# Kernel optimization log

Hardware: AMD Instinct MI355X
Metric: run time of the kernel (lower is better)

## Reference

```python
import jax, jax.numpy as jnp
import numpy as np

R = 12          # resolution (H = W = G); L = R**3 = 1728
HEADS = 12


def setup_inputs() -> dict:
    key = jax.random.key(0)
    k1, k2, k3 = jax.random.split(key, 3)
    B, L, C = 4, R ** 3, 768
    qkv = jax.random.normal(k1, (3, B, L, C), dtype=jnp.float32)
    lepe_w = jax.random.normal(k2, (C, 1, 3, 3, 3), dtype=jnp.float32) * 0.05
    lepe_b = jax.random.normal(k3, (C,), dtype=jnp.float32) * 0.01
    return {"qkv": qkv, "lepe_w": lepe_w, "lepe_b": lepe_b}


def reference(qkv, lepe_w, lepe_b):
    # qkv: [3, B, L, C]; idx=0 => window == full volume, so attention is dense over L.
    q, k, v = qkv[0], qkv[1], qkv[2]
    B, L, C = q.shape
    hd = C // HEADS
    scale = hd ** -0.5

    # im2cswin with full-volume window preserves token order: [B, L, C] -> [B, H, L, d]
    qh = q.reshape(B, L, HEADS, hd).transpose(0, 2, 1, 3)
    kh = k.reshape(B, L, HEADS, hd).transpose(0, 2, 1, 3)

    # get_lepe: v -> [B, C, R, R, R], depthwise 3x3x3 conv (groups=C)
    v_img = v.transpose(0, 2, 1).reshape(B, C, R, R, R)
    lepe = jax.lax.conv_general_dilated(
        v_img, lepe_w, window_strides=(1, 1, 1), padding="SAME",
        dimension_numbers=("NCDHW", "OIDHW", "NCDHW"), feature_group_count=C,
    ) + lepe_b[None, :, None, None, None]
    lepe = lepe.reshape(B, HEADS, hd, L).transpose(0, 1, 3, 2)   # [B, H, L, d]
    vh = v_img.reshape(B, HEADS, hd, L).transpose(0, 1, 3, 2)    # [B, H, L, d]

    attn = jax.nn.softmax(jnp.einsum("bhqd,bhkd->bhqk", qh * scale, kh), axis=-1)
    out = jnp.einsum("bhqk,bhkd->bhqd", attn, vh) + lepe          # [B, H, L, d]

    # windows2img with full window is an inverse reshape back to [B, L, C]
    return out.transpose(0, 2, 1, 3).reshape(B, L, C)
```

## Files before the change

### kernel.cpp

```cpp
#include <hip/hip_runtime.h>

#define RR 12
#define LL 1728
#define CC 768
#define HEADS 12
#define HD 64
#define BATCH 4

typedef __attribute__((ext_vector_type(8))) short bf8;
typedef __attribute__((ext_vector_type(4))) float f4;

__device__ inline unsigned short f2bf(float x) {
  unsigned int u = __float_as_uint(x);
  return (unsigned short)((u + 0x7FFFu + ((u >> 16) & 1u)) >> 16);
}
__device__ inline unsigned short f2bfr(float x) {
  return (unsigned short)((__float_as_uint(x) + 0x8000u) >> 16);
}

__device__ inline float fast_exp2(float x) {
#if __has_builtin(__builtin_amdgcn_exp2f)
  return __builtin_amdgcn_exp2f(x);
#else
  return exp2f(x);
#endif
}

__device__ inline void gld16(const unsigned short* g, unsigned short* l) {
  __builtin_amdgcn_global_load_lds((const __attribute__((address_space(1))) unsigned int*)g,
                                   (__attribute__((address_space(3))) unsigned int*)l, 16, 0, 0);
}

#define QSCALE 0.1803368801111244f

#define NLEPE 1296
#define NPREP 1296

__global__ __launch_bounds__(256) void combined_kernel(const float* __restrict__ qkv,
                                                       const float* __restrict__ w,
                                                       const float* __restrict__ bias,
                                                       unsigned short* __restrict__ qb,
                                                       unsigned short* __restrict__ kb,
                                                       unsigned short* __restrict__ vT,
                                                       float* __restrict__ out) {
  __shared__ __align__(16) unsigned char smem[27648];
  const int bid = blockIdx.x;
  const int t = threadIdx.x;

  if (bid < NLEPE) {
    const int xg = (bid % 3) * 4;
    const int yg = ((bid / 3) % 3) * 4;
    const int z = (bid / 9) % RR;
    const int ct = (bid / 108) % 3;
    const int b = bid / 324;
    const int c0 = ct * 256;
    const int c = c0 + t;
    float* w_lds = (float*)smem;

    {
      const float* wsrc = w + (size_t)c0 * 27;
#pragma unroll
      for (int i = 0; i < 7; ++i) {
        const int idx = i * 256 + t;
        if (idx < 1728) *(float4*)&w_lds[idx * 4] = *(const float4*)&wsrc[idx * 4];
      }
    }
    __syncthreads();
    float wreg[27];
#pragma unroll
    for (int j = 0; j < 27; ++j) wreg[j] = w_lds[t * 27 + j];

    const float* vb = qkv + ((size_t)(2 * BATCH + b)) * LL * CC + c;
    const float bv = bias[c];
    float acc[4][4];
#pragma unroll
    for (int yy = 0; yy < 4; ++yy)
#pragma unroll
      for (int xx = 0; xx < 4; ++xx) acc[yy][xx] = bv;

#pragma unroll
    for (int dzp = 0; dzp < 3; ++dzp) {
      const int zp = z + dzp - 1;
      const bool zok = (unsigned)zp < RR;
      float vwin[6][6];
#pragma unroll
      for (int wy = 0; wy < 6; ++wy) {
        const int yp = yg - 1 + wy;
        const bool yok = zok & ((unsigned)yp < RR);
        const int rowbase = (zp * RR + yp) * RR;
#pragma unroll
        for (int wx = 0; wx < 6; ++wx) {
          const int xp = xg - 1 + wx;
          const bool ok = yok & ((unsigned)xp < RR);
          const int lp = ok ? rowbase + xp : 0;
          const float vv = vb[(size_t)lp * CC];
          vwin[wy][wx] = ok ? vv : 0.f;
        }
      }
#pragma unroll
      for (int dy = 0; dy < 3; ++dy) {
        const float w0 = wreg[dzp * 9 + dy * 3 + 0];
        const float w1 = wreg[dzp * 9 + dy * 3 + 1];
        const float w2 = wreg[dzp * 9 + dy * 3 + 2];
#pragma unroll
        for (int yy = 0; yy < 4; ++yy) {
#pragma unroll
          for (int xx = 0; xx < 4; ++xx)
            acc[yy][xx] += w0 * vwin[yy + dy][xx] + w1 * vwin[yy + dy][xx + 1] +
                           w2 * vwin[yy + dy][xx + 2];
        }
      }
    }
#pragma unroll
    for (int yy = 0; yy < 4; ++yy) {
      const size_t obase = ((size_t)b * LL + (z * RR + yg + yy) * RR + xg) * CC + c;
#pragma unroll
      for (int xx = 0; xx < 4; ++xx) out[obase + (size_t)xx * CC] = acc[yy][xx];
    }

  } else {
    const int p = bid - NLEPE;
    const int lt = p % 27;
    const int h = (p / 27) % HEADS;
    const int b = p / (27 * HEADS);
    unsigned short* tl = (unsigned short*)smem;

    {
      const int r0 = t >> 4;
      const int c4 = (t & 15) * 4;
#pragma unroll
      for (int pi = 0; pi < 4; ++pi) {
        const int row = lt * 64 + pi * 16 + r0;
        const size_t off = ((size_t)b * LL + row) * CC + h * HD + c4;
        const float4 qv = *(const float4*)(qkv + off);
        ushort4 oq;
        oq.x = f2bf(qv.x * QSCALE); oq.y = f2bf(qv.y * QSCALE);
        oq.z = f2bf(qv.z * QSCALE); oq.w = f2bf(qv.w * QSCALE);
        *(ushort4*)(qb + off) = oq;
        const float4 kv = *(const float4*)(qkv + (size_t)BATCH * LL * CC + off);
        ushort4 ok;
        ok.x = f2bf(kv.x); ok.y = f2bf(kv.y); ok.z = f2bf(kv.z); ok.w = f2bf(kv.w);
        *(ushort4*)(kb + off) = ok;
      }
    }

    const float* vsrc = qkv + ((size_t)(2 * BATCH + b)) * LL * CC;
#pragma unroll
    for (int it = 0; it < 4; ++it) {
      const int idx = it * 256 + t;
      const int lrow = idx >> 4;
      const int c4 = (idx & 15) * 4;
      const float4 vv = *(const float4*)(vsrc + (size_t)(lt * 64 + lrow) * CC + h * HD + c4);
      tl[(c4 + 0) * 65 + lrow] = f2bf(vv.x);
      tl[(c4 + 1) * 65 + lrow] = f2bf(vv.y);
      tl[(c4 + 2) * 65 + lrow] = f2bf(vv.z);
      tl[(c4 + 3) * 65 + lrow] = f2bf(vv.w);
    }
    __syncthreads();
#pragma unroll
    for (int it = 0; it < 4; ++it) {
      const int idx = it * 256 + t;
      const int drow = idx >> 4;
      const int u = idx & 15;
      const int s4 = u * 4;
      const int kbase = (((u >> 3) * 2 + (u & 1)) << 4) + (((u >> 1) & 3) << 2);
      ushort4 o;
      o.x = tl[drow * 65 + kbase + 0];
      o.y = tl[drow * 65 + kbase + 1];
      o.z = tl[drow * 65 + kbase + 2];
      o.w = tl[drow * 65 + kbase + 3];
      *(ushort4*)(vT + (((size_t)(b * HEADS + h) * HD + drow) * LL) + lt * 64 + s4) = o;
    }
  }
}

__global__ __launch_bounds__(512, 3) void attn_kernel(const unsigned short* __restrict__ qb,
                                                      const unsigned short* __restrict__ kb,
                                                      const unsigned short* __restrict__ vT,
                                                      float* __restrict__ out) {
  __shared__ unsigned short k_lds[3][64 * 64];
  __shared__ unsigned short v_lds[3][64 * 64];

  const int g = blockIdx.x;
  const int xcd = g & 7;
  const int ix = g >> 3;
  const int qt = ix % 14;
  const int bh = xcd * 6 + ix / 14;
  const int h = bh % HEADS;
  const int b = bh / HEADS;
  const int stg = (qt * 2) % 27;

  const int t = threadIdx.x;
  const int lane = t & 63;
  const int wave = t >> 6;
  const int m = lane & 15;
  const int quad = lane >> 4;
  const int half = wave >> 2;
  const int qg = wave & 3;

  bf8 qf[2][2];
#pragma unroll
  for (int qsub = 0; qsub < 2; ++qsub) {
    int row = qt * 128 + qg * 32 + qsub * 16 + m;
    row = row < LL ? row : LL - 1;
    const size_t qbase = ((size_t)(b * LL + row)) * CC + h * HD;
    qf[qsub][0] = *(const bf8*)(qb + qbase + quad * 8);
    qf[qsub][1] = *(const bf8*)(qb + qbase + 32 + quad * 8);
  }

  int koff, voff, ldsb;
  {
    const int cidx = wave * 64 + lane;
    const int row = cidx >> 3;
    const int sc = (cidx & 7) ^ (row & 7);
    koff = row * CC + sc * 8;
    voff = row * LL + sc * 8;
    ldsb = wave * 512;
  }

  const unsigned short* kgb = kb + (size_t)b * LL * CC + h * HD;
  const unsigned short* vgb = vT + ((size_t)(b * HEADS + h) * HD) * LL;

#define ISSUE_TILE(KT, BUF)                                                             \
  {                                                                                     \
    gld16(kgb + (size_t)(KT) * (64 * CC) + koff, &k_lds[BUF][ldsb]);                    \
    gld16(vgb + (KT) * 64 + voff, &v_lds[BUF][ldsb]);                                   \
  }

  ISSUE_TILE(stg, 0)
  {
    int k1 = stg + 1; if (k1 >= 27) k1 -= 27;
    ISSUE_TILE(k1, 1)
  }

  f4 o_acc[4][2] = {};
  float psum[2] = {0.f, 0.f};

#define ATTN_BODY(I, STG, WAITN, DOISSUE)                                               \
  {                                                                                     \
    __asm__ volatile("s_waitcnt vmcnt(" #WAITN ")" ::: "memory");                       \
    __builtin_amdgcn_s_barrier();                                                       \
    if (DOISSUE) {                                                                      \
      int ktn = stg + (I) + 2; if (ktn >= 27) ktn -= 27;                                \
      ISSUE_TILE(ktn, ((STG) + 2) % 3)                                                  \
    }                                                                                   \
    f4 s_acc[2][2] = {};                            \
    __builtin_amdgcn_s_setprio(1);                                                      \
    _Pragma("unroll")                                                                   \
    for (int knt = 0; knt < 2; ++knt) {                                                 \
      _Pragma("unroll")                                                                 \
      for (int ksd = 0; ksd < 2; ++ksd) {                                               \
        const int cc = ((ksd * 4 + quad) ^ (m & 7)) * 8;                                \
        const bf8 kf = *(const bf8*)&k_lds[STG][(half * 32 + knt * 16 + m) * 64 + cc];  \
        s_acc[knt][0] = __builtin_amdgcn_mfma_f32_16x16x32_bf16(kf, qf[0][ksd], s_acc[knt][0], 0, 0, 0); \
        s_acc[knt][1] = __builtin_amdgcn_mfma_f32_16x16x32_bf16(kf, qf[1][ksd], s_acc[knt][1], 0, 0, 0); \
      }                                                                                 \
    }                                                                                   \
    __builtin_amdgcn_s_setprio(0);                                                      \
    bf8 pf[2];          \
    _Pragma("unroll")                                                                   \
    for (int qsub = 0; qsub < 2; ++qsub) {                                              \
      union { bf8 v; unsigned int w[4]; } pu;                                           \
      _Pragma("unroll")                                                                 \
      for (int knt = 0; knt < 2; ++knt) {                                               \
        const float p0 = fast_exp2(s_acc[knt][qsub][0]);                                \
        const float p1 = fast_exp2(s_acc[knt][qsub][1]);                                \
        const float p2 = fast_exp2(s_acc[knt][qsub][2]);                                \
        const float p3 = fast_exp2(s_acc[knt][qsub][3]);                                \
        psum[qsub] += (p0 + p1) + (p2 + p3);                                            \
        pu.w[knt * 2 + 0] = (unsigned int)f2bfr(p0) | ((unsigned int)f2bfr(p1) << 16);  \
        pu.w[knt * 2 + 1] = (unsigned int)f2bfr(p2) | ((unsigned int)f2bfr(p3) << 16);  \
      }                                                                                 \
      pf[qsub] = pu.v;                                                                  \
    }                                                                                   \
    __builtin_amdgcn_s_setprio(1);                                                      \
    _Pragma("unroll")                                                                   \
    for (int nt = 0; nt < 4; ++nt) {                                                    \
      const int cc = ((half * 4 + quad) ^ (m & 7)) * 8;                                 \
      const bf8 vf = *(const bf8*)&v_lds[STG][(nt * 16 + m) * 64 + cc];                 \
      o_acc[nt][0] = __builtin_amdgcn_mfma_f32_16x16x32_bf16(vf, pf[0], o_acc[nt][0], 0, 0, 0); \
      o_acc[nt][1] = __builtin_amdgcn_mfma_f32_16x16x32_bf16(vf, pf[1], o_acc[nt][1], 0, 0, 0); \
    }                                                                                   \
    __builtin_amdgcn_s_setprio(0);                                                      \
  }

  for (int ip = 0; ip < 8; ++ip) {
    const int i0 = ip * 3;
    ATTN_BODY(i0 + 0, 0, 2, true)
    ATTN_BODY(i0 + 1, 1, 2, true)
    ATTN_BODY(i0 + 2, 2, 2, true)
  }
  ATTN_BODY(24, 0, 2, true)
  ATTN_BODY(25, 1, 2, false)
  ATTN_BODY(26, 2, 0, false)
#undef ATTN_BODY
#undef ISSUE_TILE

  __syncthreads();
  {
    float* red = (float*)&k_lds[0][0];
    const int sid = qg * 64 + lane;
    float* slot = red + sid * 36;
    if (half == 1) {
#pragma unroll
      for (int qsub = 0; qsub < 2; ++qsub) {
#pragma unroll
        for (int nt = 0; nt < 4; ++nt)
          *(f4*)(slot + (qsub * 4 + nt) * 4) = o_acc[nt][qsub];
        slot[32 + qsub] = psum[qsub];
      }
    }
    __syncthreads();
    if (half == 1) return;
#pragma unroll
    for (int qsub = 0; qsub < 2; ++qsub) {
#pragma unroll
      for (int nt = 0; nt < 4; ++nt) {
        const f4 po = *(const f4*)(slot + (qsub * 4 + nt) * 4);
        o_acc[nt][qsub] += po;
      }
      psum[qsub] += slot[32 + qsub];
    }
  }

#pragma unroll
  for (int qsub = 0; qsub < 2; ++qsub) {
    float s = psum[qsub];
    s += __shfl_xor(s, 16);
    s += __shfl_xor(s, 32);
    const float inv = 1.0f / s;
    const int rowq = qt * 128 + qg * 32 + qsub * 16 + m;
    if (rowq < LL) {
      float* op = out + ((size_t)b * LL + rowq) * CC + h * HD + quad * 4;
#pragma unroll
      for (int nt = 0; nt < 4; ++nt) {
        float4 o4 = *(float4*)&op[nt * 16];
        o4.x += o_acc[nt][qsub][0] * inv;
        o4.y += o_acc[nt][qsub][1] * inv;
        o4.z += o_acc[nt][qsub][2] * inv;
        o4.w += o_acc[nt][qsub][3] * inv;
        *(float4*)&op[nt * 16] = o4;
      }
    }
  }
}

extern "C" void kernel_launch(void* const* d_in, const int* in_sizes, int n_in,
                              void* d_out, int out_size, void* d_ws, size_t ws_size,
                              hipStream_t stream) {
  (void)in_sizes; (void)n_in; (void)ws_size; (void)out_size;
  const float* qkv = (const float*)d_in[0];
  const float* lepe_w = (const float*)d_in[1];
  const float* lepe_b = (const float*)d_in[2];
  float* out = (float*)d_out;

  const size_t NE = (size_t)BATCH * LL * CC;
  unsigned short* qb = (unsigned short*)d_ws;
  unsigned short* kb = qb + NE;
  unsigned short* vT = kb + NE;

  combined_kernel<<<dim3(NLEPE + NPREP), 256, 0, stream>>>(qkv, lepe_w, lepe_b, qb, kb, vT, out);
  attn_kernel<<<dim3(672), 512, 0, stream>>>(qb, kb, vT, out);
}
```

Before: 168.7 us.

## Use double-buffered K/V LDS and split reduction to fit four blocks per CU

Moves the K/V LDS pipeline from triple to double buffering with a single merged shared array, and raises the launch bounds minimum from 3 to 4 blocks per CU. The cross-half reduction is split per qsub so its scratch fits in the smaller LDS footprint. Each iteration now waits on vmcnt(0), so only one tile is prefetched ahead. Latency hiding within a block is traded for more resident blocks, and the tighter register budget may cause spills.

```diff
diff --git a/kernel.cpp b/kernel.cpp
--- a/kernel.cpp
+++ b/kernel.cpp
@@ -174,12 +174,13 @@
   }
 }
 
-__global__ __launch_bounds__(512, 3) void attn_kernel(const unsigned short* __restrict__ qb,
+__global__ __launch_bounds__(512, 4) void attn_kernel(const unsigned short* __restrict__ qb,
                                                       const unsigned short* __restrict__ kb,
                                                       const unsigned short* __restrict__ vT,
                                                       float* __restrict__ out) {
-  __shared__ unsigned short k_lds[3][64 * 64];
-  __shared__ unsigned short v_lds[3][64 * 64];
+  __shared__ __align__(16) unsigned short smem_all[16384];
+  unsigned short* const k_base = smem_all;
+  unsigned short* const v_base = smem_all + 8192;
 
   const int g = blockIdx.x;
   const int xcd = g & 7;
@@ -223,26 +224,22 @@
 
 #define ISSUE_TILE(KT, BUF)                                                             \
   {                                                                                     \
-    gld16(kgb + (size_t)(KT) * (64 * CC) + koff, &k_lds[BUF][ldsb]);                    \
-    gld16(vgb + (KT) * 64 + voff, &v_lds[BUF][ldsb]);                                   \
+    gld16(kgb + (size_t)(KT) * (64 * CC) + koff, k_base + (BUF) * 4096 + ldsb);         \
+    gld16(vgb + (KT) * 64 + voff, v_base + (BUF) * 4096 + ldsb);                        \
   }
 
   ISSUE_TILE(stg, 0)
-  {
-    int k1 = stg + 1; if (k1 >= 27) k1 -= 27;
-    ISSUE_TILE(k1, 1)
-  }
 
   f4 o_acc[4][2] = {};
   float psum[2] = {0.f, 0.f};
 
-#define ATTN_BODY(I, STG, WAITN, DOISSUE)                                               \
+#define ATTN_BODY(I, STG, DOISSUE)                                                      \
   {                                                                                     \
-    __asm__ volatile("s_waitcnt vmcnt(" #WAITN ")" ::: "memory");                       \
+    __asm__ volatile("s_waitcnt vmcnt(0)" ::: "memory");                                \
     __builtin_amdgcn_s_barrier();                                                       \
     if (DOISSUE) {                                                                      \
-      int ktn = stg + (I) + 2; if (ktn >= 27) ktn -= 27;                                \
-      ISSUE_TILE(ktn, ((STG) + 2) % 3)                                                  \
+      int ktn = stg + (I) + 1; if (ktn >= 27) ktn -= 27;                                \
+      ISSUE_TILE(ktn, (STG) ^ 1)                                                        \
     }                                                                                   \
     f4 s_acc[2][2] = {};                            \
     __builtin_amdgcn_s_setprio(1);                                                      \
@@ -251,7 +248,7 @@
       _Pragma("unroll")                                                                 \
       for (int ksd = 0; ksd < 2; ++ksd) {                                               \
         const int cc = ((ksd * 4 + quad) ^ (m & 7)) * 8;                                \
-        const bf8 kf = *(const bf8*)&k_lds[STG][(half * 32 + knt * 16 + m) * 64 + cc];  \
+        const bf8 kf = *(const bf8*)&k_base[(STG) * 4096 + (half * 32 + knt * 16 + m) * 64 + cc]; \
         s_acc[knt][0] = __builtin_amdgcn_mfma_f32_16x16x32_bf16(kf, qf[0][ksd], s_acc[knt][0], 0, 0, 0); \
         s_acc[knt][1] = __builtin_amdgcn_mfma_f32_16x16x32_bf16(kf, qf[1][ksd], s_acc[knt][1], 0, 0, 0); \
       }                                                                                 \
@@ -277,51 +274,44 @@
     _Pragma("unroll")                                                                   \
     for (int nt = 0; nt < 4; ++nt) {                                                    \
       const int cc = ((half * 4 + quad) ^ (m & 7)) * 8;                                 \
-      const bf8 vf = *(const bf8*)&v_lds[STG][(nt * 16 + m) * 64 + cc];                 \
+      const bf8 vf = *(const bf8*)&v_base[(STG) * 4096 + (nt * 16 + m) * 64 + cc];      \
       o_acc[nt][0] = __builtin_amdgcn_mfma_f32_16x16x32_bf16(vf, pf[0], o_acc[nt][0], 0, 0, 0); \
       o_acc[nt][1] = __builtin_amdgcn_mfma_f32_16x16x32_bf16(vf, pf[1], o_acc[nt][1], 0, 0, 0); \
     }                                                                                   \
     __builtin_amdgcn_s_setprio(0);                                                      \
   }
 
-  for (int ip = 0; ip < 8; ++ip) {
-    const int i0 = ip * 3;
-    ATTN_BODY(i0 + 0, 0, 2, true)
-    ATTN_BODY(i0 + 1, 1, 2, true)
-    ATTN_BODY(i0 + 2, 2, 2, true)
-  }
-  ATTN_BODY(24, 0, 2, true)
-  ATTN_BODY(25, 1, 2, false)
-  ATTN_BODY(26, 2, 0, false)
+  for (int ip = 0; ip < 13; ++ip) {
+    const int i0 = ip * 2;
+    ATTN_BODY(i0 + 0, 0, true)
+    ATTN_BODY(i0 + 1, 1, (i0 + 1) < 26)
+  }
+  ATTN_BODY(26, 0, false)
 #undef ATTN_BODY
 #undef ISSUE_TILE
 
   __syncthreads();
   {
-    float* red = (float*)&k_lds[0][0];
+    float* red = (float*)smem_all;
     const int sid = qg * 64 + lane;
-    float* slot = red + sid * 36;
-    if (half == 1) {
-#pragma unroll
-      for (int qsub = 0; qsub < 2; ++qsub) {
-#pragma unroll
-        for (int nt = 0; nt < 4; ++nt)
-          *(f4*)(slot + (qsub * 4 + nt) * 4) = o_acc[nt][qsub];
-        slot[32 + qsub] = psum[qsub];
-      }
-    }
-    __syncthreads();
-    if (half == 1) return;
+    float* slot = red + sid * 20;
 #pragma unroll
     for (int qsub = 0; qsub < 2; ++qsub) {
-#pragma unroll
-      for (int nt = 0; nt < 4; ++nt) {
-        const f4 po = *(const f4*)(slot + (qsub * 4 + nt) * 4);
-        o_acc[nt][qsub] += po;
-      }
-      psum[qsub] += slot[32 + qsub];
-    }
-  }
+      if (half == 1) {
+#pragma unroll
+        for (int nt = 0; nt < 4; ++nt) *(f4*)(slot + nt * 4) = o_acc[nt][qsub];
+        slot[16] = psum[qsub];
+      }
+      __syncthreads();
+      if (half == 0) {
+#pragma unroll
+        for (int nt = 0; nt < 4; ++nt) o_acc[nt][qsub] += *(const f4*)(slot + nt * 4);
+        psum[qsub] += slot[16];
+      }
+      __syncthreads();
+    }
+  }
+  if (half == 1) return;
 
 #pragma unroll
   for (int qsub = 0; qsub < 2; ++qsub) {
```

Result: no change. 168.3 us (-0.3%).
